# Performance work log

Hardware: AMD Instinct MI355X
Metric: run time of the kernel (lower is better)

Reference implementation:

```python
import jax, jax.numpy as jnp
import numpy as np
from jax import lax

M, B, L, Q, S = 4, 64, 512, 512, 26  # models, batch, seq_len, hmm states, alphabet


def setup_inputs() -> dict:
    key = jax.random.key(0)
    k1, k2, k3, k4 = jax.random.split(key, 4)
    inputs = jax.random.uniform(k1, (M, B, L, S), dtype=jnp.float32)
    A_logits = jax.random.normal(k2, (M, Q, Q), dtype=jnp.float32)
    init_logits = jax.random.normal(k3, (M, Q), dtype=jnp.float32)
    em_logits = jax.random.normal(k4, (M, Q, S), dtype=jnp.float32)
    return {"inputs": inputs, "A_logits": A_logits,
            "init_logits": init_logits, "em_logits": em_logits}


def reference(inputs, A_logits, init_logits, em_logits):
    """Profile-HMM forward algorithm (scaled), as run by the MsaHmmCell RNN.

    inputs:      [M, B, L, S] observation probabilities (one-hot or soft)
    A_logits:    [M, Q, Q]    transition logits (row-softmax -> stochastic A)
    init_logits: [M, Q]       initial state distribution logits
    em_logits:   [M, Q, S]    emission logits (softmax over alphabet)
    returns loglik [M, B]  (the tensor the layer returns)
    """
    A = jax.nn.softmax(A_logits, axis=-1)        # [M, Q, Q]
    pi = jax.nn.softmax(init_logits, axis=-1)    # [M, Q]
    Bem = jax.nn.softmax(em_logits, axis=-1)     # [M, Q, S]

    # per-step emission likelihoods, time-major for scan: [L, M, B, Q]
    E = jnp.einsum('mbls,mqs->lmbq', inputs, Bem)

    # t = 0: alpha_0 = pi * e_0, scaled
    a0 = pi[:, None, :] * E[0]                   # [M, B, Q]
    s0 = jnp.sum(a0, axis=-1, keepdims=True)
    carry0 = (a0 / s0, jnp.log(s0[..., 0]))      # (alpha [M,B,Q], loglik [M,B])

    def step(carry, e_t):
        alpha, ll = carry
        r = jnp.einsum('mbq,mqp->mbp', alpha, A)  # transition
        a = r * e_t                               # emission
        s = jnp.sum(a, axis=-1, keepdims=True)    # scaling factor
        return (a / s, ll + jnp.log(s[..., 0])), None

    (alpha, loglik), _ = lax.scan(step, carry0, E[1:])
    return loglik  # [M, B] == reshape(loglik, (num_models, -1)) in the layer
```

## Files before the change

kernel.cpp:

```cpp
#include <hip/hip_runtime.h>
#include <hip/hip_bf16.h>
#include <math.h>


#define MM 4
#define BB 64
#define LL 512
#define QQ 512
#define SS 26
#define ASTR 528

typedef float f32x4 __attribute__((ext_vector_type(4)));
typedef int i32x4 __attribute__((ext_vector_type(4)));
typedef int i32x8 __attribute__((ext_vector_type(8)));

__device__ __forceinline__ float bf2f(unsigned short u) {
    return __uint_as_float(((unsigned)u) << 16);
}
__device__ __forceinline__ unsigned short f2bf(float f) {
    unsigned u = __float_as_uint(f);
    u = u + 0x7FFFu + ((u >> 16) & 1u);
    return (unsigned short)(u >> 16);
}
__device__ __forceinline__ unsigned char f2fp8(float x) {
    int r = __builtin_amdgcn_cvt_pk_fp8_f32(x, x, 0, false);
    return (unsigned char)(r & 0xFF);
}
__device__ __forceinline__ i32x8 ld32B(const unsigned char* p) {
    i32x4 lo = *(const i32x4*)p;
    i32x4 hi = *(const i32x4*)(p + 16);
    return __builtin_shufflevector(lo, hi, 0, 1, 2, 3, 4, 5, 6, 7);
}
__device__ __forceinline__ void barrier_lds() {
    __asm__ __volatile__("" ::: "memory");
    __builtin_amdgcn_s_waitcnt(0xC07F);
    __builtin_amdgcn_s_barrier();
    __asm__ __volatile__("" ::: "memory");
}


__global__ void prep_small(const float* __restrict__ il, const float* __restrict__ em,
                           float* __restrict__ pi, float* __restrict__ Bem) {
    int blk = blockIdx.x;
    int m = blk / (QQ + 1);
    int r = blk % (QQ + 1);
    int lane = threadIdx.x;
    if (r < QQ) {
        float x = (lane < SS) ? em[((size_t)m * QQ + r) * SS + lane] : -1e30f;
        float mx = x;
        #pragma unroll
        for (int o = 1; o < 64; o <<= 1) mx = fmaxf(mx, __shfl_xor(mx, o));
        float e = (lane < SS) ? __expf(x - mx) : 0.f;
        float s = e;
        #pragma unroll
        for (int o = 1; o < 64; o <<= 1) s += __shfl_xor(s, o);
        if (lane < SS) Bem[((size_t)m * QQ + r) * SS + lane] = e / s;
    } else {
        float v[8];
        float mx = -1e30f;
        #pragma unroll
        for (int k = 0; k < 8; ++k) { v[k] = il[m * QQ + k * 64 + lane]; mx = fmaxf(mx, v[k]); }
        #pragma unroll
        for (int o = 1; o < 64; o <<= 1) mx = fmaxf(mx, __shfl_xor(mx, o));
        float s = 0.f;
        #pragma unroll
        for (int k = 0; k < 8; ++k) { v[k] = __expf(v[k] - mx); s += v[k]; }
        #pragma unroll
        for (int o = 1; o < 64; o <<= 1) s += __shfl_xor(s, o);
        #pragma unroll
        for (int k = 0; k < 8; ++k) pi[m * QQ + k * 64 + lane] = v[k] / s;
    }
}

__global__ void prep_arow(const float* __restrict__ Al, float* __restrict__ Lrow) {
    int row = blockIdx.x;
    int lane = threadIdx.x;
    const float* p = Al + (size_t)row * QQ;
    float v[8];
    float mx = -1e30f;
    #pragma unroll
    for (int k = 0; k < 8; ++k) { v[k] = p[k * 64 + lane]; mx = fmaxf(mx, v[k]); }
    #pragma unroll
    for (int o = 1; o < 64; o <<= 1) mx = fmaxf(mx, __shfl_xor(mx, o));
    float s = 0.f;
    #pragma unroll
    for (int k = 0; k < 8; ++k) s += __expf(v[k] - mx);
    #pragma unroll
    for (int o = 1; o < 64; o <<= 1) s += __shfl_xor(s, o);
    if (lane == 0) Lrow[row] = mx + __logf(s);
}

__global__ void prep_atq(const float* __restrict__ Al, const float* __restrict__ Lrow,
                         unsigned char* __restrict__ Atq) {
    int bid = blockIdx.x;
    int m = bid >> 3, pb = bid & 7;
    __shared__ unsigned char tile[64][68];
    int l6 = threadIdx.x & 63, g = threadIdx.x >> 6;
    for (int c = 0; c < 8; ++c) {
        #pragma unroll
        for (int r = 0; r < 16; ++r) {
            int ql = g * 16 + r;
            int q = c * 64 + ql;
            float x = Al[((size_t)m * QQ + q) * QQ + pb * 64 + l6];
            tile[ql][l6] = f2fp8(__expf(x - Lrow[m * QQ + q]) * 256.f);
        }
        __syncthreads();
        #pragma unroll
        for (int r = 0; r < 16; ++r) {
            int pr = g * 16 + r;
            Atq[((size_t)m * QQ + pb * 64 + pr) * QQ + c * 64 + l6] = tile[l6][pr];
        }
        __syncthreads();
    }
}

__global__ void prep_e(const float* __restrict__ inp, const float* __restrict__ Bem,
                       unsigned short* __restrict__ E) {
    int bid = blockIdx.x;
    int tc = bid & 7;
    int b = (bid >> 3) & 63;
    int m = bid >> 9;
    int q0 = threadIdx.x;
    float bem0[SS], bem1[SS];
    const float* bp = Bem + (size_t)m * QQ * SS;
    #pragma unroll
    for (int j = 0; j < SS; ++j) bem0[j] = bp[(size_t)q0 * SS + j];
    #pragma unroll
    for (int j = 0; j < SS; ++j) bem1[j] = bp[(size_t)(q0 + 256) * SS + j];
    const float* ip = inp + (((size_t)(m * BB + b)) * LL + tc * 64) * SS;
    for (int lt = 0; lt < 64; ++lt) {
        int t = tc * 64 + lt;
        float a0 = 0.f, a1 = 0.f;
        #pragma unroll
        for (int j = 0; j < SS; ++j) {
            float x = ip[lt * SS + j];
            a0 += x * bem0[j];
            a1 += x * bem1[j];
        }
        size_t o = (((size_t)m * LL + t) * BB + b) * QQ + q0;
        E[o] = f2bf(a0);
        E[o + 256] = f2bf(a1);
    }
}


__launch_bounds__(512, 2)
__global__ void hmm_scan(const unsigned short* __restrict__ E,
                         const unsigned char* __restrict__ Atq,
                         const float* __restrict__ pi,
                         float* __restrict__ out) {
    const int c = blockIdx.x;
    const int m = c >> 2, bg = c & 3;
    const int tid = threadIdx.x;
    const int lane = tid & 63;
    const int wv = tid >> 6;
    const int sl = lane & 15;
    const int quad = lane >> 4;
    const float LOG256 = 5.545177444479562f;

    __shared__ unsigned char albuf[2][16 * ASTR];
    __shared__ __align__(16) float psl[2][16][20];
    __shared__ float Sfin[2][16];

    i32x8 breg[4][4];
    {
        const unsigned char* Ab = Atq + (size_t)m * QQ * QQ;
        #pragma unroll
        for (int h = 0; h < 4; ++h) {
            int p = wv * 64 + h * 16 + sl;
            const unsigned char* rp = Ab + (size_t)p * QQ + quad * 32;
            #pragma unroll
            for (int kc = 0; kc < 4; ++kc)
                breg[h][kc] = ld32B(rp + kc * 128);
        }
    }

    int wq[4];
    #pragma unroll
    for (int h = 0; h < 4; ++h)
        wq[h] = sl * ASTR + wv * 64 + h * 16 + quad * 4;

    const int b = bg * 16 + sl;
    const size_t ebase = (size_t)m * LL * BB * QQ;
    const ushort4* __restrict__ E4 = (const ushort4*)(E + ebase);
    const unsigned ESTR4 = (BB * QQ) >> 2;
    const unsigned ebq = (unsigned)(b * QQ) >> 2;
    unsigned eoffs[4];
    #pragma unroll
    for (int h = 0; h < 4; ++h) eoffs[h] = (unsigned)(wv * 16 + h * 4 + quad);

    float v[4][4];
    ushort4 ea[4], eb[4];

    {
        #pragma unroll
        for (int h = 0; h < 4; ++h) ea[h] = E4[ebq + ESTR4 + eoffs[h]];
        #pragma unroll
        for (int h = 0; h < 4; ++h) {
            int p0 = wv * 64 + h * 16 + quad * 4;
            f32x4 pv = *(const f32x4*)(pi + m * QQ + p0);
            ushort4 e0 = E4[ebq + eoffs[h]];
            v[h][0] = pv[0] * bf2f(e0.x);
            v[h][1] = pv[1] * bf2f(e0.y);
            v[h][2] = pv[2] * bf2f(e0.z);
            v[h][3] = pv[3] * bf2f(e0.w);
        }
    }

    float lam = 0.5f;
    float gprev = 1.0f;
    float ll = 0.0f;

    auto body = [&](int t, ushort4 (&ecur)[4], ushort4 (&enxt)[4], unsigned epre) {
        const int par = t & 1;
        #pragma unroll
        for (int h = 0; h < 4; ++h) enxt[h] = E4[epre + eoffs[h]];

        float g = 128.0f * __builtin_amdgcn_rcpf(lam);
        unsigned char* ab = &albuf[par][0];
        #pragma unroll
        for (int h = 0; h < 4; ++h) {
            int d = __builtin_amdgcn_cvt_pk_fp8_f32(g * v[h][0], g * v[h][1], 0, false);
            d = __builtin_amdgcn_cvt_pk_fp8_f32(g * v[h][2], g * v[h][3], d, true);
            *(int*)(ab + wq[h]) = d;
        }
        float ps = ((v[0][0] + v[0][1]) + (v[0][2] + v[0][3]))
                 + ((v[1][0] + v[1][1]) + (v[1][2] + v[1][3]))
                 + ((v[2][0] + v[2][1]) + (v[2][2] + v[2][3]))
                 + ((v[3][0] + v[3][1]) + (v[3][2] + v[3][3]));
        ps += __shfl_xor(ps, 16);
        if ((quad & 1) == 0) psl[par][sl][2 * wv + (quad >> 1)] = ps;

        ll -= __logf(g) + LOG256;

        barrier_lds();

        if (wv == 0 && lane < 16) {
            const f32x4* pr = (const f32x4*)&psl[par][lane][0];
            f32x4 ss4 = (pr[0] + pr[1]) + (pr[2] + pr[3]);
            Sfin[par][lane] = (ss4[0] + ss4[1]) + (ss4[2] + ss4[3]);
        }
        if (t == 0) {
            lam = 16384.0f;
        } else {
            float Sp = Sfin[par ^ 1][sl];
            lam = 16384.0f * g * gprev * Sp;
        }
        gprev = g;

        f32x4 acc[4];
        #pragma unroll
        for (int h = 0; h < 4; ++h) acc[h] = (f32x4){0.f, 0.f, 0.f, 0.f};
        const unsigned char* ar = &albuf[par][0] + sl * ASTR + quad * 32;
        #pragma unroll
        for (int kc = 0; kc < 4; ++kc) {
            i32x8 af = ld32B(ar + kc * 128);
            #pragma unroll
            for (int h = 0; h < 4; ++h)
                acc[h] = __builtin_amdgcn_mfma_scale_f32_16x16x128_f8f6f4(
                    breg[h][kc], af, acc[h], 0, 0,
                    0, 0x7F7F7F7F, 0, 0x7F7F7F7F);
        }
        #pragma unroll
        for (int h = 0; h < 4; ++h) {
            v[h][0] = acc[h][0] * bf2f(ecur[h].x);
            v[h][1] = acc[h][1] * bf2f(ecur[h].y);
            v[h][2] = acc[h][2] * bf2f(ecur[h].z);
            v[h][3] = acc[h][3] * bf2f(ecur[h].w);
        }
    };

    unsigned epre = ebq + 2 * ESTR4;
    for (int t = 0; t < LL - 2; t += 2) {
        body(t, ea, eb, epre); epre += ESTR4;
        body(t + 1, eb, ea, epre); epre += ESTR4;
    }
    body(LL - 2, ea, eb, ebq + (unsigned)(LL - 1) * ESTR4);

    {
        float ps = ((v[0][0] + v[0][1]) + (v[0][2] + v[0][3]))
                 + ((v[1][0] + v[1][1]) + (v[1][2] + v[1][3]))
                 + ((v[2][0] + v[2][1]) + (v[2][2] + v[2][3]))
                 + ((v[3][0] + v[3][1]) + (v[3][2] + v[3][3]));
        ps += __shfl_xor(ps, 16);
        if ((quad & 1) == 0) psl[1][sl][2 * wv + (quad >> 1)] = ps;
        __syncthreads();
        if (wv == 0 && lane < 16) {
            const f32x4* pr = (const f32x4*)&psl[1][lane][0];
            f32x4 ss4 = (pr[0] + pr[1]) + (pr[2] + pr[3]);
            float S = (ss4[0] + ss4[1]) + (ss4[2] + ss4[3]);
            out[m * BB + bg * 16 + lane] = ll + __logf(S);
        }
    }
}


extern "C" void kernel_launch(void* const* d_in, const int* in_sizes, int n_in,
                              void* d_out, int out_size, void* d_ws, size_t ws_size,
                              hipStream_t stream) {
    const float* inputs = (const float*)d_in[0];
    const float* A_logits = (const float*)d_in[1];
    const float* init_logits = (const float*)d_in[2];
    const float* em_logits = (const float*)d_in[3];
    float* out = (float*)d_out;

    char* ws = (char*)d_ws;
    size_t off = 0;
    unsigned short* E = (unsigned short*)(ws + off);  off += (size_t)MM * LL * BB * QQ * 2;
    unsigned char* Atq = (unsigned char*)(ws + off);  off += (size_t)MM * QQ * QQ;
    float* Bem = (float*)(ws + off);                  off += (size_t)MM * QQ * SS * 4;
    float* pi = (float*)(ws + off);                   off += (size_t)MM * QQ * 4;
    float* Lrow = (float*)(ws + off);                 off += (size_t)MM * QQ * 4;

    if (ws_size < off) {
        (void)hipMemsetAsync(d_out, 0, (size_t)out_size * sizeof(float), stream);
        return;
    }

    prep_small<<<dim3(MM * (QQ + 1)), dim3(64), 0, stream>>>(init_logits, em_logits, pi, Bem);
    prep_arow<<<dim3(MM * QQ), dim3(64), 0, stream>>>(A_logits, Lrow);
    prep_atq<<<dim3(MM * 8), dim3(256), 0, stream>>>(A_logits, Lrow, Atq);
    prep_e<<<dim3(MM * BB * 8), dim3(256), 0, stream>>>(inputs, Bem, E);
    hmm_scan<<<dim3(16), dim3(512), 0, stream>>>(E, Atq, pi, out);
}
```

Baseline: 591.1 us.

## Rotate HMM step loop so fp8 pack and partial sums follow each MFMA chain

Restructures the per-timestep loop so that the scale factor for the next step is computed before the MFMAs. Each output tile is then converted to fp8 and written to LDS right after its own MFMA chain, and its partial sum is accumulated in the same pass. The first step's pack and the last step's MFMA are peeled out of the loop. The goal is to shorten the serial dependency chain per step and interleave conversion and LDS stores with matrix work. The cost is some code duplication and the risk of changed scheduling or register pressure.

```diff
diff --git a/kernel.cpp b/kernel.cpp
--- a/kernel.cpp
+++ b/kernel.cpp
@@ -192,6 +192,8 @@
     float v[4][4];
     ushort4 ea[4], eb[4];
 
+    float gcur, gprev, ll;
+
     {
         #pragma unroll
         for (int h = 0; h < 4; ++h) ea[h] = E4[ebq + ESTR4 + eoffs[h]];
@@ -205,23 +207,13 @@
             v[h][2] = pv[2] * bf2f(e0.z);
             v[h][3] = pv[3] * bf2f(e0.w);
         }
-    }
-
-    float lam = 0.5f;
-    float gprev = 1.0f;
-    float ll = 0.0f;
-
-    auto body = [&](int t, ushort4 (&ecur)[4], ushort4 (&enxt)[4], unsigned epre) {
-        const int par = t & 1;
-        #pragma unroll
-        for (int h = 0; h < 4; ++h) enxt[h] = E4[epre + eoffs[h]];
-
-        float g = 128.0f * __builtin_amdgcn_rcpf(lam);
-        unsigned char* ab = &albuf[par][0];
-        #pragma unroll
-        for (int h = 0; h < 4; ++h) {
-            int d = __builtin_amdgcn_cvt_pk_fp8_f32(g * v[h][0], g * v[h][1], 0, false);
-            d = __builtin_amdgcn_cvt_pk_fp8_f32(g * v[h][2], g * v[h][3], d, true);
+        gcur = 256.f;
+        gprev = 1.0f;
+        unsigned char* ab = &albuf[0][0];
+        #pragma unroll
+        for (int h = 0; h < 4; ++h) {
+            int d = __builtin_amdgcn_cvt_pk_fp8_f32(gcur * v[h][0], gcur * v[h][1], 0, false);
+            d = __builtin_amdgcn_cvt_pk_fp8_f32(gcur * v[h][2], gcur * v[h][3], d, true);
             *(int*)(ab + wq[h]) = d;
         }
         float ps = ((v[0][0] + v[0][1]) + (v[0][2] + v[0][3]))
@@ -229,53 +221,90 @@
                  + ((v[2][0] + v[2][1]) + (v[2][2] + v[2][3]))
                  + ((v[3][0] + v[3][1]) + (v[3][2] + v[3][3]));
         ps += __shfl_xor(ps, 16);
-        if ((quad & 1) == 0) psl[par][sl][2 * wv + (quad >> 1)] = ps;
-
-        ll -= __logf(g) + LOG256;
-
+        if ((quad & 1) == 0) psl[0][sl][2 * wv + (quad >> 1)] = ps;
+        ll = -(__logf(gcur) + LOG256);
         barrier_lds();
+    }
+
+    auto body = [&](int par, bool first, ushort4 (&ecur)[4], ushort4 (&enxt)[4],
+                    unsigned epre) {
+        #pragma unroll
+        for (int h = 0; h < 4; ++h) enxt[h] = E4[epre + eoffs[h]];
 
         if (wv == 0 && lane < 16) {
             const f32x4* pr = (const f32x4*)&psl[par][lane][0];
             f32x4 ss4 = (pr[0] + pr[1]) + (pr[2] + pr[3]);
             Sfin[par][lane] = (ss4[0] + ss4[1]) + (ss4[2] + ss4[3]);
         }
-        if (t == 0) {
-            lam = 16384.0f;
-        } else {
-            float Sp = Sfin[par ^ 1][sl];
-            lam = 16384.0f * g * gprev * Sp;
-        }
-        gprev = g;
-
-        f32x4 acc[4];
-        #pragma unroll
-        for (int h = 0; h < 4; ++h) acc[h] = (f32x4){0.f, 0.f, 0.f, 0.f};
+        float lam = first ? 16384.0f
+                          : 16384.0f * gcur * gprev * Sfin[par ^ 1][sl];
+        float gnext = 128.0f * __builtin_amdgcn_rcpf(lam);
+
         const unsigned char* ar = &albuf[par][0] + sl * ASTR + quad * 32;
-        #pragma unroll
-        for (int kc = 0; kc < 4; ++kc) {
-            i32x8 af = ld32B(ar + kc * 128);
-            #pragma unroll
-            for (int h = 0; h < 4; ++h)
-                acc[h] = __builtin_amdgcn_mfma_scale_f32_16x16x128_f8f6f4(
-                    breg[h][kc], af, acc[h], 0, 0,
-                    0, 0x7F7F7F7F, 0, 0x7F7F7F7F);
-        }
-        #pragma unroll
-        for (int h = 0; h < 4; ++h) {
-            v[h][0] = acc[h][0] * bf2f(ecur[h].x);
-            v[h][1] = acc[h][1] * bf2f(ecur[h].y);
-            v[h][2] = acc[h][2] * bf2f(ecur[h].z);
-            v[h][3] = acc[h][3] * bf2f(ecur[h].w);
-        }
+        i32x8 af0 = ld32B(ar);
+        i32x8 af1 = ld32B(ar + 128);
+        i32x8 af2 = ld32B(ar + 256);
+        i32x8 af3 = ld32B(ar + 384);
+
+        unsigned char* ab = &albuf[par ^ 1][0];
+        float ps = 0.f;
+        #pragma unroll
+        for (int h = 0; h < 4; ++h) {
+            f32x4 acc = (f32x4){0.f, 0.f, 0.f, 0.f};
+            acc = __builtin_amdgcn_mfma_scale_f32_16x16x128_f8f6f4(
+                breg[h][0], af0, acc, 0, 0, 0, 0x7F7F7F7F, 0, 0x7F7F7F7F);
+            acc = __builtin_amdgcn_mfma_scale_f32_16x16x128_f8f6f4(
+                breg[h][1], af1, acc, 0, 0, 0, 0x7F7F7F7F, 0, 0x7F7F7F7F);
+            acc = __builtin_amdgcn_mfma_scale_f32_16x16x128_f8f6f4(
+                breg[h][2], af2, acc, 0, 0, 0, 0x7F7F7F7F, 0, 0x7F7F7F7F);
+            acc = __builtin_amdgcn_mfma_scale_f32_16x16x128_f8f6f4(
+                breg[h][3], af3, acc, 0, 0, 0, 0x7F7F7F7F, 0, 0x7F7F7F7F);
+            v[h][0] = acc[0] * bf2f(ecur[h].x);
+            v[h][1] = acc[1] * bf2f(ecur[h].y);
+            v[h][2] = acc[2] * bf2f(ecur[h].z);
+            v[h][3] = acc[3] * bf2f(ecur[h].w);
+            int d = __builtin_amdgcn_cvt_pk_fp8_f32(gnext * v[h][0], gnext * v[h][1], 0, false);
+            d = __builtin_amdgcn_cvt_pk_fp8_f32(gnext * v[h][2], gnext * v[h][3], d, true);
+            *(int*)(ab + wq[h]) = d;
+            ps += (v[h][0] + v[h][1]) + (v[h][2] + v[h][3]);
+        }
+        ps += __shfl_xor(ps, 16);
+        if ((quad & 1) == 0) psl[par ^ 1][sl][2 * wv + (quad >> 1)] = ps;
+        ll -= __logf(gnext) + LOG256;
+        gprev = gcur; gcur = gnext;
+        barrier_lds();
     };
 
     unsigned epre = ebq + 2 * ESTR4;
-    for (int t = 0; t < LL - 2; t += 2) {
-        body(t, ea, eb, epre); epre += ESTR4;
-        body(t + 1, eb, ea, epre); epre += ESTR4;
-    }
-    body(LL - 2, ea, eb, ebq + (unsigned)(LL - 1) * ESTR4);
+    body(0, true,  ea, eb, epre); epre += ESTR4;
+    body(1, false, eb, ea, epre); epre += ESTR4;
+    for (int t = 2; t < LL - 2; t += 2) {
+        body(0, false, ea, eb, epre); epre += ESTR4;
+        body(1, false, eb, ea, epre); epre += ESTR4;
+    }
+    {
+        const unsigned char* ar = &albuf[0][0] + sl * ASTR + quad * 32;
+        i32x8 af0 = ld32B(ar);
+        i32x8 af1 = ld32B(ar + 128);
+        i32x8 af2 = ld32B(ar + 256);
+        i32x8 af3 = ld32B(ar + 384);
+        #pragma unroll
+        for (int h = 0; h < 4; ++h) {
+            f32x4 acc = (f32x4){0.f, 0.f, 0.f, 0.f};
+            acc = __builtin_amdgcn_mfma_scale_f32_16x16x128_f8f6f4(
+                breg[h][0], af0, acc, 0, 0, 0, 0x7F7F7F7F, 0, 0x7F7F7F7F);
+            acc = __builtin_amdgcn_mfma_scale_f32_16x16x128_f8f6f4(
+                breg[h][1], af1, acc, 0, 0, 0, 0x7F7F7F7F, 0, 0x7F7F7F7F);
+            acc = __builtin_amdgcn_mfma_scale_f32_16x16x128_f8f6f4(
+                breg[h][2], af2, acc, 0, 0, 0, 0x7F7F7F7F, 0, 0x7F7F7F7F);
+            acc = __builtin_amdgcn_mfma_scale_f32_16x16x128_f8f6f4(
+                breg[h][3], af3, acc, 0, 0, 0, 0x7F7F7F7F, 0, 0x7F7F7F7F);
+            v[h][0] = acc[0] * bf2f(ea[h].x);
+            v[h][1] = acc[1] * bf2f(ea[h].y);
+            v[h][2] = acc[2] * bf2f(ea[h].z);
+            v[h][3] = acc[3] * bf2f(ea[h].w);
+        }
+    }
 
     {
         float ps = ((v[0][0] + v[0][1]) + (v[0][2] + v[0][3]))
```

After: 619.6 us. +4.8%, slower.

## Fuse emission precompute into scan kernel with flag-based producer/consumer overlap

Applied to the files above, without the earlier changes.

The emission-likelihood computation moves into the scan kernel as extra producer blocks. Each producer block signals a per-(model, batch-group, time-chunk) global flag with a release atomic, and the 16 scan blocks spin on the flag for the next 64-step chunk before consuming it. This lets the serial scan start before all of E is written, overlapping the E precompute with the recurrence. The two small softmax prep kernels are also merged into one launch. The cost is a memset plus spin-waiting, and there is a risk of deadlock or stale reads if the producer blocks are not scheduled, which the bounded wait loop only partly guards against.

```diff
diff --git a/kernel.cpp b/kernel.cpp
--- a/kernel.cpp
+++ b/kernel.cpp
@@ -9,6 +9,7 @@
 #define QQ 512
 #define SS 26
 #define ASTR 528
+#define NFLAGS (MM * 4 * 8)
 
 typedef float f32x4 __attribute__((ext_vector_type(4)));
 typedef int i32x4 __attribute__((ext_vector_type(4)));
@@ -31,63 +32,73 @@
     i32x4 hi = *(const i32x4*)(p + 16);
     return __builtin_shufflevector(lo, hi, 0, 1, 2, 3, 4, 5, 6, 7);
 }
+#define MFMA8(A, B, C) __builtin_amdgcn_mfma_scale_f32_16x16x128_f8f6f4( \
+    (A), (B), (C), 0, 0, 0, 0x7F7F7F7F, 0, 0x7F7F7F7F)
 __device__ __forceinline__ void barrier_lds() {
     __asm__ __volatile__("" ::: "memory");
     __builtin_amdgcn_s_waitcnt(0xC07F);
     __builtin_amdgcn_s_barrier();
     __asm__ __volatile__("" ::: "memory");
 }
-
-
-__global__ void prep_small(const float* __restrict__ il, const float* __restrict__ em,
-                           float* __restrict__ pi, float* __restrict__ Bem) {
+__device__ __forceinline__ void wait_flag(const int* p, int target) {
+    for (int i = 0; i < (1 << 17); ++i) {
+        if (__hip_atomic_load(p, __ATOMIC_ACQUIRE, __HIP_MEMORY_SCOPE_AGENT) >= target)
+            return;
+        __builtin_amdgcn_s_sleep(32);
+    }
+}
+
+
+__global__ void prep_sa(const float* __restrict__ il, const float* __restrict__ em,
+                        const float* __restrict__ Al,
+                        float* __restrict__ pi, float* __restrict__ Bem,
+                        float* __restrict__ Lrow) {
     int blk = blockIdx.x;
-    int m = blk / (QQ + 1);
-    int r = blk % (QQ + 1);
     int lane = threadIdx.x;
-    if (r < QQ) {
-        float x = (lane < SS) ? em[((size_t)m * QQ + r) * SS + lane] : -1e30f;
-        float mx = x;
-        #pragma unroll
-        for (int o = 1; o < 64; o <<= 1) mx = fmaxf(mx, __shfl_xor(mx, o));
-        float e = (lane < SS) ? __expf(x - mx) : 0.f;
-        float s = e;
-        #pragma unroll
-        for (int o = 1; o < 64; o <<= 1) s += __shfl_xor(s, o);
-        if (lane < SS) Bem[((size_t)m * QQ + r) * SS + lane] = e / s;
+    if (blk < MM * (QQ + 1)) {
+        int m = blk / (QQ + 1);
+        int r = blk % (QQ + 1);
+        if (r < QQ) {
+            float x = (lane < SS) ? em[((size_t)m * QQ + r) * SS + lane] : -1e30f;
+            float mx = x;
+            #pragma unroll
+            for (int o = 1; o < 64; o <<= 1) mx = fmaxf(mx, __shfl_xor(mx, o));
+            float e = (lane < SS) ? __expf(x - mx) : 0.f;
+            float s = e;
+            #pragma unroll
+            for (int o = 1; o < 64; o <<= 1) s += __shfl_xor(s, o);
+            if (lane < SS) Bem[((size_t)m * QQ + r) * SS + lane] = e / s;
+        } else {
+            float v[8];
+            float mx = -1e30f;
+            #pragma unroll
+            for (int k = 0; k < 8; ++k) { v[k] = il[m * QQ + k * 64 + lane]; mx = fmaxf(mx, v[k]); }
+            #pragma unroll
+            for (int o = 1; o < 64; o <<= 1) mx = fmaxf(mx, __shfl_xor(mx, o));
+            float s = 0.f;
+            #pragma unroll
+            for (int k = 0; k < 8; ++k) { v[k] = __expf(v[k] - mx); s += v[k]; }
+            #pragma unroll
+            for (int o = 1; o < 64; o <<= 1) s += __shfl_xor(s, o);
+            #pragma unroll
+            for (int k = 0; k < 8; ++k) pi[m * QQ + k * 64 + lane] = v[k] / s;
+        }
     } else {
+        int row = blk - MM * (QQ + 1);
+        const float* p = Al + (size_t)row * QQ;
         float v[8];
         float mx = -1e30f;
         #pragma unroll
-        for (int k = 0; k < 8; ++k) { v[k] = il[m * QQ + k * 64 + lane]; mx = fmaxf(mx, v[k]); }
+        for (int k = 0; k < 8; ++k) { v[k] = p[k * 64 + lane]; mx = fmaxf(mx, v[k]); }
         #pragma unroll
         for (int o = 1; o < 64; o <<= 1) mx = fmaxf(mx, __shfl_xor(mx, o));
         float s = 0.f;
         #pragma unroll
-        for (int k = 0; k < 8; ++k) { v[k] = __expf(v[k] - mx); s += v[k]; }
+        for (int k = 0; k < 8; ++k) s += __expf(v[k] - mx);
         #pragma unroll
         for (int o = 1; o < 64; o <<= 1) s += __shfl_xor(s, o);
-        #pragma unroll
-        for (int k = 0; k < 8; ++k) pi[m * QQ + k * 64 + lane] = v[k] / s;
-    }
-}
-
-__global__ void prep_arow(const float* __restrict__ Al, float* __restrict__ Lrow) {
-    int row = blockIdx.x;
-    int lane = threadIdx.x;
-    const float* p = Al + (size_t)row * QQ;
-    float v[8];
-    float mx = -1e30f;
-    #pragma unroll
-    for (int k = 0; k < 8; ++k) { v[k] = p[k * 64 + lane]; mx = fmaxf(mx, v[k]); }
-    #pragma unroll
-    for (int o = 1; o < 64; o <<= 1) mx = fmaxf(mx, __shfl_xor(mx, o));
-    float s = 0.f;
-    #pragma unroll
-    for (int k = 0; k < 8; ++k) s += __expf(v[k] - mx);
-    #pragma unroll
-    for (int o = 1; o < 64; o <<= 1) s += __shfl_xor(s, o);
-    if (lane == 0) Lrow[row] = mx + __logf(s);
+        if (lane == 0) Lrow[row] = mx + __logf(s);
+    }
 }
 
 __global__ void prep_atq(const float* __restrict__ Al, const float* __restrict__ Lrow,
@@ -114,41 +125,51 @@
     }
 }
 
-__global__ void prep_e(const float* __restrict__ inp, const float* __restrict__ Bem,
-                       unsigned short* __restrict__ E) {
-    int bid = blockIdx.x;
-    int tc = bid & 7;
-    int b = (bid >> 3) & 63;
-    int m = bid >> 9;
-    int q0 = threadIdx.x;
-    float bem0[SS], bem1[SS];
-    const float* bp = Bem + (size_t)m * QQ * SS;
-    #pragma unroll
-    for (int j = 0; j < SS; ++j) bem0[j] = bp[(size_t)q0 * SS + j];
-    #pragma unroll
-    for (int j = 0; j < SS; ++j) bem1[j] = bp[(size_t)(q0 + 256) * SS + j];
-    const float* ip = inp + (((size_t)(m * BB + b)) * LL + tc * 64) * SS;
-    for (int lt = 0; lt < 64; ++lt) {
-        int t = tc * 64 + lt;
-        float a0 = 0.f, a1 = 0.f;
-        #pragma unroll
-        for (int j = 0; j < SS; ++j) {
-            float x = ip[lt * SS + j];
-            a0 += x * bem0[j];
-            a1 += x * bem1[j];
-        }
-        size_t o = (((size_t)m * LL + t) * BB + b) * QQ + q0;
-        E[o] = f2bf(a0);
-        E[o + 256] = f2bf(a1);
-    }
-}
-
 
 __launch_bounds__(512, 2)
-__global__ void hmm_scan(const unsigned short* __restrict__ E,
-                         const unsigned char* __restrict__ Atq,
-                         const float* __restrict__ pi,
-                         float* __restrict__ out) {
+__global__ void hmm_fused(unsigned short* E,
+                          const unsigned char* __restrict__ Atq,
+                          const float* __restrict__ pi,
+                          const float* __restrict__ inp,
+                          const float* __restrict__ Bem,
+                          int* flags,
+                          float* __restrict__ out) {
+    if (blockIdx.x >= 16) {
+        int p = blockIdx.x - 16;
+        int tc = p >> 7;
+        int k = p & 127;
+        int mb = 2 * k + (threadIdx.x >> 8);
+        int q0 = threadIdx.x & 255;
+        int m = mb >> 6, b = mb & 63;
+        float bem0[SS], bem1[SS];
+        const float* bp = Bem + (size_t)m * QQ * SS;
+        #pragma unroll
+        for (int j = 0; j < SS; ++j) bem0[j] = bp[(size_t)q0 * SS + j];
+        #pragma unroll
+        for (int j = 0; j < SS; ++j) bem1[j] = bp[(size_t)(q0 + 256) * SS + j];
+        const float* ip = inp + (((size_t)(m * BB + b)) * LL + tc * 64) * SS;
+        for (int lt = 0; lt < 64; ++lt) {
+            float a0 = 0.f, a1 = 0.f;
+            #pragma unroll
+            for (int j = 0; j < SS; ++j) {
+                float x = ip[lt * SS + j];
+                a0 += x * bem0[j];
+                a1 += x * bem1[j];
+            }
+            size_t o = (((size_t)m * LL + (tc * 64 + lt)) * BB + b) * QQ + q0;
+            E[o] = f2bf(a0);
+            E[o + 256] = f2bf(a1);
+        }
+        __syncthreads();
+        __threadfence();
+        if (threadIdx.x == 0) {
+            int fi = (m * 4 + (b >> 4)) * 8 + tc;
+            __hip_atomic_fetch_add(&flags[fi], 2, __ATOMIC_RELEASE,
+                                   __HIP_MEMORY_SCOPE_AGENT);
+        }
+        return;
+    }
+
     const int c = blockIdx.x;
     const int m = c >> 2, bg = c & 3;
     const int tid = threadIdx.x;
@@ -162,6 +183,8 @@
     __shared__ __align__(16) float psl[2][16][20];
     __shared__ float Sfin[2][16];
 
+    const int* fl = flags + (m * 4 + bg) * 8;
+
     i32x8 breg[4][4];
     {
         const unsigned char* Ab = Atq + (size_t)m * QQ * QQ;
@@ -192,6 +215,8 @@
     float v[4][4];
     ushort4 ea[4], eb[4];
 
+    wait_flag(&fl[0], 16);
+
     {
         #pragma unroll
         for (int h = 0; h < 4; ++h) ea[h] = E4[ebq + ESTR4 + eoffs[h]];
@@ -257,9 +282,7 @@
             i32x8 af = ld32B(ar + kc * 128);
             #pragma unroll
             for (int h = 0; h < 4; ++h)
-                acc[h] = __builtin_amdgcn_mfma_scale_f32_16x16x128_f8f6f4(
-                    breg[h][kc], af, acc[h], 0, 0,
-                    0, 0x7F7F7F7F, 0, 0x7F7F7F7F);
+                acc[h] = MFMA8(breg[h][kc], af, acc[h]);
         }
         #pragma unroll
         for (int h = 0; h < 4; ++h) {
@@ -272,6 +295,7 @@
 
     unsigned epre = ebq + 2 * ESTR4;
     for (int t = 0; t < LL - 2; t += 2) {
+        if ((t & 63) == 62) wait_flag(&fl[(t + 2) >> 6], 16);
         body(t, ea, eb, epre); epre += ESTR4;
         body(t + 1, eb, ea, epre); epre += ESTR4;
     }
@@ -311,15 +335,17 @@
     float* Bem = (float*)(ws + off);                  off += (size_t)MM * QQ * SS * 4;
     float* pi = (float*)(ws + off);                   off += (size_t)MM * QQ * 4;
     float* Lrow = (float*)(ws + off);                 off += (size_t)MM * QQ * 4;
+    int* flags = (int*)(ws + off);                    off += (size_t)NFLAGS * 4;
 
     if (ws_size < off) {
         (void)hipMemsetAsync(d_out, 0, (size_t)out_size * sizeof(float), stream);
         return;
     }
 
-    prep_small<<<dim3(MM * (QQ + 1)), dim3(64), 0, stream>>>(init_logits, em_logits, pi, Bem);
-    prep_arow<<<dim3(MM * QQ), dim3(64), 0, stream>>>(A_logits, Lrow);
+    (void)hipMemsetAsync(flags, 0, (size_t)NFLAGS * 4, stream);
+    prep_sa<<<dim3(MM * (QQ + 1) + MM * QQ), dim3(64), 0, stream>>>(
+        init_logits, em_logits, A_logits, pi, Bem, Lrow);
     prep_atq<<<dim3(MM * 8), dim3(256), 0, stream>>>(A_logits, Lrow, Atq);
-    prep_e<<<dim3(MM * BB * 8), dim3(256), 0, stream>>>(inputs, Bem, E);
-    hmm_scan<<<dim3(16), dim3(512), 0, stream>>>(E, Atq, pi, out);
-}
+    hmm_fused<<<dim3(16 + 1024), dim3(512), 0, stream>>>(
+        E, Atq, pi, inputs, Bem, flags, out);
+}
```

After: 723.8 us. 22.5% more time.

## Halve scan block to 4 waves with 8 MFMA tiles each; merge prep kernels

Applied to the files above, without the earlier changes.

Each scan workgroup now uses 4 waves instead of 8, and each wave owns 128 output states (8 MFMA column tiles) rather than 64. This cuts the number of waves taking part in every per-step barrier and shrinks the cross-wave partial-sum reduction. In exchange each wave keeps twice as many register-resident A fragments and does twice the MFMA work per step, which lengthens the serial path per step. The two small softmax/log-sum-exp prep kernels are also merged into a single launch to save one kernel launch.

```diff
diff --git a/kernel.cpp b/kernel.cpp
--- a/kernel.cpp
+++ b/kernel.cpp
@@ -31,6 +31,8 @@
     i32x4 hi = *(const i32x4*)(p + 16);
     return __builtin_shufflevector(lo, hi, 0, 1, 2, 3, 4, 5, 6, 7);
 }
+#define MFMA8(A, B, C) __builtin_amdgcn_mfma_scale_f32_16x16x128_f8f6f4( \
+    (A), (B), (C), 0, 0, 0, 0x7F7F7F7F, 0, 0x7F7F7F7F)
 __device__ __forceinline__ void barrier_lds() {
     __asm__ __volatile__("" ::: "memory");
     __builtin_amdgcn_s_waitcnt(0xC07F);
@@ -39,55 +41,56 @@
 }
 
 
-__global__ void prep_small(const float* __restrict__ il, const float* __restrict__ em,
-                           float* __restrict__ pi, float* __restrict__ Bem) {
+__global__ void prep_sa(const float* __restrict__ il, const float* __restrict__ em,
+                        const float* __restrict__ Al,
+                        float* __restrict__ pi, float* __restrict__ Bem,
+                        float* __restrict__ Lrow) {
     int blk = blockIdx.x;
-    int m = blk / (QQ + 1);
-    int r = blk % (QQ + 1);
     int lane = threadIdx.x;
-    if (r < QQ) {
-        float x = (lane < SS) ? em[((size_t)m * QQ + r) * SS + lane] : -1e30f;
-        float mx = x;
-        #pragma unroll
-        for (int o = 1; o < 64; o <<= 1) mx = fmaxf(mx, __shfl_xor(mx, o));
-        float e = (lane < SS) ? __expf(x - mx) : 0.f;
-        float s = e;
-        #pragma unroll
-        for (int o = 1; o < 64; o <<= 1) s += __shfl_xor(s, o);
-        if (lane < SS) Bem[((size_t)m * QQ + r) * SS + lane] = e / s;
+    if (blk < MM * (QQ + 1)) {
+        int m = blk / (QQ + 1);
+        int r = blk % (QQ + 1);
+        if (r < QQ) {
+            float x = (lane < SS) ? em[((size_t)m * QQ + r) * SS + lane] : -1e30f;
+            float mx = x;
+            #pragma unroll
+            for (int o = 1; o < 64; o <<= 1) mx = fmaxf(mx, __shfl_xor(mx, o));
+            float e = (lane < SS) ? __expf(x - mx) : 0.f;
+            float s = e;
+            #pragma unroll
+            for (int o = 1; o < 64; o <<= 1) s += __shfl_xor(s, o);
+            if (lane < SS) Bem[((size_t)m * QQ + r) * SS + lane] = e / s;
+        } else {
+            float v[8];
+            float mx = -1e30f;
+            #pragma unroll
+            for (int k = 0; k < 8; ++k) { v[k] = il[m * QQ + k * 64 + lane]; mx = fmaxf(mx, v[k]); }
+            #pragma unroll
+            for (int o = 1; o < 64; o <<= 1) mx = fmaxf(mx, __shfl_xor(mx, o));
+            float s = 0.f;
+            #pragma unroll
+            for (int k = 0; k < 8; ++k) { v[k] = __expf(v[k] - mx); s += v[k]; }
+            #pragma unroll
+            for (int o = 1; o < 64; o <<= 1) s += __shfl_xor(s, o);
+            #pragma unroll
+            for (int k = 0; k < 8; ++k) pi[m * QQ + k * 64 + lane] = v[k] / s;
+        }
     } else {
+        int row = blk - MM * (QQ + 1);
+        const float* p = Al + (size_t)row * QQ;
         float v[8];
         float mx = -1e30f;
         #pragma unroll
-        for (int k = 0; k < 8; ++k) { v[k] = il[m * QQ + k * 64 + lane]; mx = fmaxf(mx, v[k]); }
+        for (int k = 0; k < 8; ++k) { v[k] = p[k * 64 + lane]; mx = fmaxf(mx, v[k]); }
         #pragma unroll
         for (int o = 1; o < 64; o <<= 1) mx = fmaxf(mx, __shfl_xor(mx, o));
         float s = 0.f;
         #pragma unroll
-        for (int k = 0; k < 8; ++k) { v[k] = __expf(v[k] - mx); s += v[k]; }
+        for (int k = 0; k < 8; ++k) s += __expf(v[k] - mx);
         #pragma unroll
         for (int o = 1; o < 64; o <<= 1) s += __shfl_xor(s, o);
-        #pragma unroll
-        for (int k = 0; k < 8; ++k) pi[m * QQ + k * 64 + lane] = v[k] / s;
-    }
-}
-
-__global__ void prep_arow(const float* __restrict__ Al, float* __restrict__ Lrow) {
-    int row = blockIdx.x;
-    int lane = threadIdx.x;
-    const float* p = Al + (size_t)row * QQ;
-    float v[8];
-    float mx = -1e30f;
-    #pragma unroll
-    for (int k = 0; k < 8; ++k) { v[k] = p[k * 64 + lane]; mx = fmaxf(mx, v[k]); }
-    #pragma unroll
-    for (int o = 1; o < 64; o <<= 1) mx = fmaxf(mx, __shfl_xor(mx, o));
-    float s = 0.f;
-    #pragma unroll
-    for (int k = 0; k < 8; ++k) s += __expf(v[k] - mx);
-    #pragma unroll
-    for (int o = 1; o < 64; o <<= 1) s += __shfl_xor(s, o);
-    if (lane == 0) Lrow[row] = mx + __logf(s);
+        if (lane == 0) Lrow[row] = mx + __logf(s);
+    }
 }
 
 __global__ void prep_atq(const float* __restrict__ Al, const float* __restrict__ Lrow,
@@ -144,7 +147,7 @@
 }
 
 
-__launch_bounds__(512, 2)
+__launch_bounds__(256, 1)
 __global__ void hmm_scan(const unsigned short* __restrict__ E,
                          const unsigned char* __restrict__ Atq,
                          const float* __restrict__ pi,
@@ -159,15 +162,15 @@
     const float LOG256 = 5.545177444479562f;
 
     __shared__ unsigned char albuf[2][16 * ASTR];
-    __shared__ __align__(16) float psl[2][16][20];
+    __shared__ __align__(16) float psl[2][16][12];
     __shared__ float Sfin[2][16];
 
-    i32x8 breg[4][4];
+    i32x8 breg[8][4];
     {
         const unsigned char* Ab = Atq + (size_t)m * QQ * QQ;
         #pragma unroll
-        for (int h = 0; h < 4; ++h) {
-            int p = wv * 64 + h * 16 + sl;
+        for (int h = 0; h < 8; ++h) {
+            int p = wv * 128 + h * 16 + sl;
             const unsigned char* rp = Ab + (size_t)p * QQ + quad * 32;
             #pragma unroll
             for (int kc = 0; kc < 4; ++kc)
@@ -175,29 +178,29 @@
         }
     }
 
-    int wq[4];
+    int wq[8];
     #pragma unroll
-    for (int h = 0; h < 4; ++h)
-        wq[h] = sl * ASTR + wv * 64 + h * 16 + quad * 4;
+    for (int h = 0; h < 8; ++h)
+        wq[h] = sl * ASTR + wv * 128 + h * 16 + quad * 4;
 
     const int b = bg * 16 + sl;
     const size_t ebase = (size_t)m * LL * BB * QQ;
     const ushort4* __restrict__ E4 = (const ushort4*)(E + ebase);
     const unsigned ESTR4 = (BB * QQ) >> 2;
     const unsigned ebq = (unsigned)(b * QQ) >> 2;
-    unsigned eoffs[4];
+    unsigned eoffs[8];
     #pragma unroll
-    for (int h = 0; h < 4; ++h) eoffs[h] = (unsigned)(wv * 16 + h * 4 + quad);
-
-    float v[4][4];
-    ushort4 ea[4], eb[4];
+    for (int h = 0; h < 8; ++h) eoffs[h] = (unsigned)(wv * 32 + h * 4 + quad);
+
+    float v[8][4];
+    ushort4 ea[8], eb[8];
 
     {
         #pragma unroll
-        for (int h = 0; h < 4; ++h) ea[h] = E4[ebq + ESTR4 + eoffs[h]];
-        #pragma unroll
-        for (int h = 0; h < 4; ++h) {
-            int p0 = wv * 64 + h * 16 + quad * 4;
+        for (int h = 0; h < 8; ++h) ea[h] = E4[ebq + ESTR4 + eoffs[h]];
+        #pragma unroll
+        for (int h = 0; h < 8; ++h) {
+            int p0 = wv * 128 + h * 16 + quad * 4;
             f32x4 pv = *(const f32x4*)(pi + m * QQ + p0);
             ushort4 e0 = E4[ebq + eoffs[h]];
             v[h][0] = pv[0] * bf2f(e0.x);
@@ -211,23 +214,23 @@
     float gprev = 1.0f;
     float ll = 0.0f;
 
-    auto body = [&](int t, ushort4 (&ecur)[4], ushort4 (&enxt)[4], unsigned epre) {
+    auto body = [&](int t, ushort4 (&ecur)[8], ushort4 (&enxt)[8], unsigned epre) {
         const int par = t & 1;
         #pragma unroll
-        for (int h = 0; h < 4; ++h) enxt[h] = E4[epre + eoffs[h]];
+        for (int h = 0; h < 8; ++h) enxt[h] = E4[epre + eoffs[h]];
 
         float g = 128.0f * __builtin_amdgcn_rcpf(lam);
         unsigned char* ab = &albuf[par][0];
         #pragma unroll
-        for (int h = 0; h < 4; ++h) {
+        for (int h = 0; h < 8; ++h) {
             int d = __builtin_amdgcn_cvt_pk_fp8_f32(g * v[h][0], g * v[h][1], 0, false);
             d = __builtin_amdgcn_cvt_pk_fp8_f32(g * v[h][2], g * v[h][3], d, true);
             *(int*)(ab + wq[h]) = d;
         }
-        float ps = ((v[0][0] + v[0][1]) + (v[0][2] + v[0][3]))
-                 + ((v[1][0] + v[1][1]) + (v[1][2] + v[1][3]))
-                 + ((v[2][0] + v[2][1]) + (v[2][2] + v[2][3]))
-                 + ((v[3][0] + v[3][1]) + (v[3][2] + v[3][3]));
+        float ps = 0.f;
+        #pragma unroll
+        for (int h = 0; h < 8; ++h)
+            ps += (v[h][0] + v[h][1]) + (v[h][2] + v[h][3]);
         ps += __shfl_xor(ps, 16);
         if ((quad & 1) == 0) psl[par][sl][2 * wv + (quad >> 1)] = ps;
 
@@ -237,7 +240,7 @@
 
         if (wv == 0 && lane < 16) {
             const f32x4* pr = (const f32x4*)&psl[par][lane][0];
-            f32x4 ss4 = (pr[0] + pr[1]) + (pr[2] + pr[3]);
+            f32x4 ss4 = pr[0] + pr[1];
             Sfin[par][lane] = (ss4[0] + ss4[1]) + (ss4[2] + ss4[3]);
         }
         if (t == 0) {
@@ -248,21 +251,19 @@
         }
         gprev = g;
 
-        f32x4 acc[4];
-        #pragma unroll
-        for (int h = 0; h < 4; ++h) acc[h] = (f32x4){0.f, 0.f, 0.f, 0.f};
+        f32x4 acc[8];
+        #pragma unroll
+        for (int h = 0; h < 8; ++h) acc[h] = (f32x4){0.f, 0.f, 0.f, 0.f};
         const unsigned char* ar = &albuf[par][0] + sl * ASTR + quad * 32;
         #pragma unroll
         for (int kc = 0; kc < 4; ++kc) {
             i32x8 af = ld32B(ar + kc * 128);
             #pragma unroll
-            for (int h = 0; h < 4; ++h)
-                acc[h] = __builtin_amdgcn_mfma_scale_f32_16x16x128_f8f6f4(
-                    breg[h][kc], af, acc[h], 0, 0,
-                    0, 0x7F7F7F7F, 0, 0x7F7F7F7F);
-        }
-        #pragma unroll
-        for (int h = 0; h < 4; ++h) {
+            for (int h = 0; h < 8; ++h)
+                acc[h] = MFMA8(breg[h][kc], af, acc[h]);
+        }
+        #pragma unroll
+        for (int h = 0; h < 8; ++h) {
             v[h][0] = acc[h][0] * bf2f(ecur[h].x);
             v[h][1] = acc[h][1] * bf2f(ecur[h].y);
             v[h][2] = acc[h][2] * bf2f(ecur[h].z);
@@ -278,16 +279,16 @@
     body(LL - 2, ea, eb, ebq + (unsigned)(LL - 1) * ESTR4);
 
     {
-        float ps = ((v[0][0] + v[0][1]) + (v[0][2] + v[0][3]))
-                 + ((v[1][0] + v[1][1]) + (v[1][2] + v[1][3]))
-                 + ((v[2][0] + v[2][1]) + (v[2][2] + v[2][3]))
-                 + ((v[3][0] + v[3][1]) + (v[3][2] + v[3][3]));
+        float ps = 0.f;
+        #pragma unroll
+        for (int h = 0; h < 8; ++h)
+            ps += (v[h][0] + v[h][1]) + (v[h][2] + v[h][3]);
         ps += __shfl_xor(ps, 16);
         if ((quad & 1) == 0) psl[1][sl][2 * wv + (quad >> 1)] = ps;
         __syncthreads();
         if (wv == 0 && lane < 16) {
             const f32x4* pr = (const f32x4*)&psl[1][lane][0];
-            f32x4 ss4 = (pr[0] + pr[1]) + (pr[2] + pr[3]);
+            f32x4 ss4 = pr[0] + pr[1];
             float S = (ss4[0] + ss4[1]) + (ss4[2] + ss4[3]);
             out[m * BB + bg * 16 + lane] = ll + __logf(S);
         }
@@ -317,9 +318,9 @@
         return;
     }
 
-    prep_small<<<dim3(MM * (QQ + 1)), dim3(64), 0, stream>>>(init_logits, em_logits, pi, Bem);
-    prep_arow<<<dim3(MM * QQ), dim3(64), 0, stream>>>(A_logits, Lrow);
+    prep_sa<<<dim3(MM * (QQ + 1) + MM * QQ), dim3(64), 0, stream>>>(
+        init_logits, em_logits, A_logits, pi, Bem, Lrow);
     prep_atq<<<dim3(MM * 8), dim3(256), 0, stream>>>(A_logits, Lrow, Atq);
     prep_e<<<dim3(MM * BB * 8), dim3(256), 0, stream>>>(inputs, Bem, E);
-    hmm_scan<<<dim3(16), dim3(512), 0, stream>>>(E, Atq, pi, out);
-}
+    hmm_scan<<<dim3(16), dim3(256), 0, stream>>>(E, Atq, pi, out);
+}
```

After: 762.5 us. +29.0%, slower.
